# Optimization experiments

Measured on AMD Instinct MI355X. Metric: run time of the kernel, lower is better.

## Reference

```python
import jax, jax.numpy as jnp
import numpy as np

N_AGENTS, OBS_DIM, HID, ACT_DIM = 8192, 64, 128, 16


def setup_inputs() -> dict:
    key = jax.random.key(0)
    k = jax.random.split(key, 8)
    obs_agents = jax.random.normal(k[0], (N_AGENTS, OBS_DIM), dtype=jnp.float32)
    # binary adjacency, {0,1}, int32 (index/mask semantics, non-differentiable)
    adj = jax.random.randint(k[1], (N_AGENTS, N_AGENTS), 0, 2, dtype=jnp.int32)
    def lin(kk, fan_in, fan_out):
        lim = 1.0 / np.sqrt(fan_in)
        kw, kb = jax.random.split(kk)
        W = jax.random.uniform(kw, (fan_in, fan_out), jnp.float32, -lim, lim)
        b = jax.random.uniform(kb, (fan_out,), jnp.float32, -lim, lim)
        return W, b
    W1, b1 = lin(k[2], OBS_DIM, HID)          # encoder
    W2, b2 = lin(k[3], 2 * HID, HID)          # actor layer 1
    W3, b3 = lin(k[4], HID, ACT_DIM)          # actor layer 2
    return {"obs_agents": obs_agents, "adj": adj,
            "W1": W1, "b1": b1, "W2": W2, "b2": b2, "W3": W3, "b3": b3}


def reference(obs_agents, adj, W1, b1, W2, b2, W3, b3):
    # per-agent encode: h = tanh(obs @ W1 + b1)  -> [N, HID]
    h = jnp.tanh(obs_agents @ W1 + b1)
    # neighbor mean message: mean of h[j] over j with adj[i,j]!=0, zeros if no neighbors
    a = adj.astype(h.dtype)                      # [N, N] binary
    deg = jnp.sum(a, axis=1, keepdims=True)      # [N, 1]
    msg = (a @ h) / jnp.maximum(deg, 1.0)        # zero rows stay zero
    # actor MLP on concat([h, msg])
    combined = jnp.concatenate([h, msg], axis=-1)            # [N, 2*HID]
    hid = jnp.tanh(combined @ W2 + b2)                        # [N, HID]
    logits = hid @ W3 + b3                                    # [N, ACT_DIM]
    return logits
```

## Files before the change

### kernel.cpp

```cpp
#include <hip/hip_runtime.h>
#include <stdint.h>
#include <math.h>

#define NAG 8192
#define NB  144
#define BM  128
#define NSPLIT 32
#define LDB 264

typedef __attribute__((ext_vector_type(8))) short short8;
typedef __attribute__((ext_vector_type(4))) float floatx4;

__device__ __forceinline__ float bf2f(unsigned short u) {
    union { uint32_t i; float f; } v; v.i = ((uint32_t)u) << 16; return v.f;
}
__device__ __forceinline__ unsigned short f2bf(float f) {
    union { float f; uint32_t i; } v; v.f = f;
    uint32_t x = v.i;
    return (unsigned short)((x + 0x7FFFu + ((x >> 16) & 1u)) >> 16);
}
__device__ __forceinline__ unsigned short f2h(float f) {
    union { _Float16 h; unsigned short u; } v; v.h = (_Float16)f; return v.u;
}
__device__ __forceinline__ float h2f(unsigned short u) {
    union { _Float16 h; unsigned short u; } v; v.u = u; return (float)v.h;
}

__global__ __launch_bounds__(64) void k0_init(
    int* __restrict__ flag, const unsigned short* __restrict__ W1raw)
{
    int big = 0;
    #pragma unroll
    for (int j = 0; j < 8; ++j) {
        float v = bf2f(W1raw[threadIdx.x * 8 + j]);
        if (!(fabsf(v) <= 1e6f)) big = 1;
    }
    unsigned long long m = __ballot(big);
    if (threadIdx.x == 0) *flag = (m != 0ull) ? 1 : 0;
}

__global__ __launch_bounds__(256) void k1_encode(
    const void* __restrict__ obs,
    const void* __restrict__ W1,
    const void* __restrict__ b1,
    const int* __restrict__ flag,
    float* __restrict__ h_f32,
    unsigned short* __restrict__ hT)
{
    __shared__ float obs_lds[32][68];
    __shared__ unsigned short ht_lds[128][33];
    const int t = threadIdx.x;
    const int abase = blockIdx.x * 32;
    const bool isf = (*flag != 0);

    {
        int a = t >> 3, c0 = (t & 7) * 8;
        if (isf) {
            const float* p = (const float*)obs;
            #pragma unroll
            for (int j = 0; j < 8; ++j)
                obs_lds[a][c0 + j] = p[(size_t)(abase + a) * 64 + c0 + j];
        } else {
            const unsigned short* p = (const unsigned short*)obs;
            #pragma unroll
            for (int j = 0; j < 8; ++j)
                obs_lds[a][c0 + j] = bf2f(p[(size_t)(abase + a) * 64 + c0 + j]);
        }
    }
    __syncthreads();

    const int o = t & 127;
    const int half = t >> 7;
    float acc[16];
    if (isf) {
        const float* Wp = (const float*)W1;
        float bias = ((const float*)b1)[o];
        #pragma unroll
        for (int i = 0; i < 16; ++i) acc[i] = bias;
        for (int k0 = 0; k0 < 64; k0 += 8) {
            float w[8];
            #pragma unroll
            for (int j = 0; j < 8; ++j) w[j] = Wp[(k0 + j) * 128 + o];
            #pragma unroll
            for (int j = 0; j < 8; ++j)
                #pragma unroll
                for (int i = 0; i < 16; ++i)
                    acc[i] = fmaf(obs_lds[half * 16 + i][k0 + j], w[j], acc[i]);
        }
    } else {
        const unsigned short* Wp = (const unsigned short*)W1;
        float bias = bf2f(((const unsigned short*)b1)[o]);
        #pragma unroll
        for (int i = 0; i < 16; ++i) acc[i] = bias;
        for (int k0 = 0; k0 < 64; k0 += 8) {
            float w[8];
            #pragma unroll
            for (int j = 0; j < 8; ++j) w[j] = bf2f(Wp[(k0 + j) * 128 + o]);
            #pragma unroll
            for (int j = 0; j < 8; ++j)
                #pragma unroll
                for (int i = 0; i < 16; ++i)
                    acc[i] = fmaf(obs_lds[half * 16 + i][k0 + j], w[j], acc[i]);
        }
    }
    #pragma unroll
    for (int i = 0; i < 16; ++i) {
        float th = tanhf(acc[i]);
        int a = half * 16 + i;
        h_f32[(size_t)(abase + a) * 128 + o] = th;
        ht_lds[o][a] = f2bf(th);
    }
    __syncthreads();

    for (int p = 0; p < 18; ++p) {
        int n = p * 8 + (t >> 5);
        int a = t & 31;
        unsigned short v;
        if (n < 128)       v = ht_lds[n][a];
        else if (n == 128) v = 0x3F80;
        else               v = 0;
        hT[(size_t)n * NAG + abase + a] = v;
    }
}

__global__ __launch_bounds__(512, 4) void k2_msggemm(
    const int* __restrict__ adj,
    const unsigned short* __restrict__ hT,
    unsigned short* __restrict__ Cp16)
{
    __shared__ __align__(16) unsigned short Blds[144 * LDB];
    const int t = threadIdx.x;
    const int mtile = blockIdx.x & 63;
    const int ks = blockIdx.x >> 6;
    const int row0 = mtile * BM;
    const int kbeg = ks * 256;

    const int wave = t >> 6, lane = t & 63;
    const int fm = lane & 15, quad = lane >> 4;

    #pragma unroll
    for (int i = 0; i < 9; ++i) {
        int idx = i * 512 + t;
        int row = idx >> 5, ch = idx & 31;
        uint4 v = *reinterpret_cast<const uint4*>(hT + (size_t)row * NAG + kbeg + ch * 8);
        *reinterpret_cast<uint4*>(&Blds[row * LDB + ch * 8]) = v;
    }
    __syncthreads();

    floatx4 acc[9];
    #pragma unroll
    for (int i = 0; i < 9; ++i) acc[i] = (floatx4)0.f;

    const int* aP = adj + (size_t)(row0 + wave * 16 + fm) * NAG + kbeg + quad * 8;

    for (int w = 0; w < 8; ++w) {
        int4 v0 = *reinterpret_cast<const int4*>(aP + w * 32);
        int4 v1 = *reinterpret_cast<const int4*>(aP + w * 32 + 4);
        union { uint32_t u[4]; short8 s; } af;
        af.u[0] = ((uint32_t)v0.x | ((uint32_t)v0.y << 16)) * 0x3F80u;
        af.u[1] = ((uint32_t)v0.z | ((uint32_t)v0.w << 16)) * 0x3F80u;
        af.u[2] = ((uint32_t)v1.x | ((uint32_t)v1.y << 16)) * 0x3F80u;
        af.u[3] = ((uint32_t)v1.z | ((uint32_t)v1.w << 16)) * 0x3F80u;
        #pragma unroll
        for (int j = 0; j < 9; ++j) {
            short8 bf = *reinterpret_cast<const short8*>(&Blds[(j * 16 + fm) * LDB + w * 32 + quad * 8]);
            acc[j] = __builtin_amdgcn_mfma_f32_16x16x32_bf16(af.s, bf, acc[j], 0, 0, 0);
        }
    }

    unsigned short* out = Cp16 + (size_t)ks * (NAG * NB);
    #pragma unroll
    for (int j = 0; j < 9; ++j) {
        int col = j * 16 + fm;
        #pragma unroll
        for (int r = 0; r < 4; ++r) {
            int row = row0 + wave * 16 + quad * 4 + r;
            out[(size_t)row * NB + col] = f2h(acc[j][r]);
        }
    }
}

__global__ __launch_bounds__(256) void k3_actor(
    const float* __restrict__ h_f32,
    const unsigned short* __restrict__ Cp16,
    const void* __restrict__ W2,
    const void* __restrict__ b2,
    const void* __restrict__ W3,
    const void* __restrict__ b3,
    const int* __restrict__ flag,
    void* __restrict__ out)
{
    __shared__ float4 comb4[16][66];
    __shared__ float hid[16][132];
    __shared__ float inv_lds[16];
    const int t = threadIdx.x;
    const int abase = blockIdx.x * 16;
    const bool isf = (*flag != 0);
    const size_t PS = (size_t)NAG * NB;

    if (t < 16) {
        float deg = 0.f;
        #pragma unroll
        for (int s = 0; s < NSPLIT; ++s)
            deg += h2f(Cp16[s * PS + (size_t)(abase + t) * NB + 128]);
        inv_lds[t] = 1.0f / fmaxf(deg, 1.0f);
    }
    __syncthreads();

    #pragma unroll
    for (int jj = 0; jj < 4; ++jj) {
        int idx = jj * 256 + t;
        int a = idx >> 6, q = idx & 63;
        float4 v;
        if (q < 32) {
            v = *reinterpret_cast<const float4*>(h_f32 + (size_t)(abase + a) * 128 + q * 4);
        } else {
            int f = (q - 32) * 4;
            float s0 = 0.f, s1 = 0.f, s2 = 0.f, s3 = 0.f;
            #pragma unroll
            for (int s = 0; s < NSPLIT; ++s) {
                ushort4 p = *reinterpret_cast<const ushort4*>(Cp16 + s * PS + (size_t)(abase + a) * NB + f);
                s0 += h2f(p.x); s1 += h2f(p.y); s2 += h2f(p.z); s3 += h2f(p.w);
            }
            float sc = inv_lds[a];
            v = make_float4(s0 * sc, s1 * sc, s2 * sc, s3 * sc);
        }
        comb4[a][q] = v;
    }
    __syncthreads();

    const int o = t & 127, half = t >> 7;
    float acc[8];
    if (isf) {
        const float* Wp = (const float*)W2;
        float bias = ((const float*)b2)[o];
        #pragma unroll
        for (int i = 0; i < 8; ++i) acc[i] = bias;
        for (int cq = 0; cq < 64; ++cq) {
            float w0 = Wp[(cq * 4 + 0) * 128 + o];
            float w1 = Wp[(cq * 4 + 1) * 128 + o];
            float w2 = Wp[(cq * 4 + 2) * 128 + o];
            float w3 = Wp[(cq * 4 + 3) * 128 + o];
            #pragma unroll
            for (int i = 0; i < 8; ++i) {
                float4 v = comb4[half * 8 + i][cq];
                acc[i] = fmaf(v.x, w0, acc[i]);
                acc[i] = fmaf(v.y, w1, acc[i]);
                acc[i] = fmaf(v.z, w2, acc[i]);
                acc[i] = fmaf(v.w, w3, acc[i]);
            }
        }
    } else {
        const unsigned short* Wp = (const unsigned short*)W2;
        float bias = bf2f(((const unsigned short*)b2)[o]);
        #pragma unroll
        for (int i = 0; i < 8; ++i) acc[i] = bias;
        for (int cq = 0; cq < 64; ++cq) {
            float w0 = bf2f(Wp[(cq * 4 + 0) * 128 + o]);
            float w1 = bf2f(Wp[(cq * 4 + 1) * 128 + o]);
            float w2 = bf2f(Wp[(cq * 4 + 2) * 128 + o]);
            float w3 = bf2f(Wp[(cq * 4 + 3) * 128 + o]);
            #pragma unroll
            for (int i = 0; i < 8; ++i) {
                float4 v = comb4[half * 8 + i][cq];
                acc[i] = fmaf(v.x, w0, acc[i]);
                acc[i] = fmaf(v.y, w1, acc[i]);
                acc[i] = fmaf(v.z, w2, acc[i]);
                acc[i] = fmaf(v.w, w3, acc[i]);
            }
        }
    }
    #pragma unroll
    for (int i = 0; i < 8; ++i)
        hid[half * 8 + i][o] = tanhf(acc[i]);
    __syncthreads();

    const int q = t & 15, ar = t >> 4;
    float l;
    if (isf) {
        const float* Wp = (const float*)W3;
        l = ((const float*)b3)[q];
        #pragma unroll 4
        for (int oo = 0; oo < 128; ++oo)
            l = fmaf(hid[ar][oo], Wp[oo * 16 + q], l);
    } else {
        const unsigned short* Wp = (const unsigned short*)W3;
        l = bf2f(((const unsigned short*)b3)[q]);
        #pragma unroll 4
        for (int oo = 0; oo < 128; ++oo)
            l = fmaf(hid[ar][oo], bf2f(Wp[oo * 16 + q]), l);
    }
    size_t i0 = (size_t)(abase + ar) * 16 + q;
    if (isf) ((float*)out)[i0] = l;
    else     ((unsigned short*)out)[i0] = f2bf(l);
}

extern "C" void kernel_launch(void* const* d_in, const int* in_sizes, int n_in,
                              void* d_out, int out_size, void* d_ws, size_t ws_size,
                              hipStream_t stream) {
    const void* obs = d_in[0];
    const int*  adj = (const int*)d_in[1];
    const void* W1  = d_in[2];
    const void* b1  = d_in[3];
    const void* W2  = d_in[4];
    const void* b2  = d_in[5];
    const void* W3  = d_in[6];
    const void* b3  = d_in[7];

    char* ws = (char*)d_ws;
    unsigned short* hT   = (unsigned short*)(ws);
    float*          h_f32= (float*)(ws + 2359296);
    unsigned short* Cp16 = (unsigned short*)(ws + 6553600);
    int*            flag = (int*)(ws + 82051072);

    hipLaunchKernelGGL(k0_init, dim3(1), dim3(64), 0, stream, flag, (const unsigned short*)W1);
    hipLaunchKernelGGL(k1_encode, dim3(256), dim3(256), 0, stream, obs, W1, b1, flag, h_f32, hT);
    hipLaunchKernelGGL(k2_msggemm, dim3(2048), dim3(512), 0, stream, adj, hT, Cp16);
    hipLaunchKernelGGL(k3_actor, dim3(512), dim3(256), 0, stream, h_f32, Cp16, W2, b2, W3, b3, flag, d_out);
}
```

Baseline: 457.8 us.

## Stage adjacency tile in LDS and stream hT from global in msg GEMM

Swaps which operand of the adjacency-times-h GEMM is staged in shared memory. The int32 adjacency tile is now loaded coalesced, converted to bf16 and stored in LDS, while the hT operand is read directly from global memory (cached) per MFMA. The M tile halves to 64 rows with 256-thread blocks, doubling the grid, to cut LDS size and raise occupancy. The change trades a coalesced adj load for uncoalesced per-lane global reads of hT that are repeated across blocks.

```diff
diff --git a/kernel.cpp b/kernel.cpp
--- a/kernel.cpp
+++ b/kernel.cpp
@@ -4,9 +4,10 @@
 
 #define NAG 8192
 #define NB  144
-#define BM  128
+#define BM  64
+#define BK  256
 #define NSPLIT 32
-#define LDB 264
+#define LDA 264
 
 typedef __attribute__((ext_vector_type(8))) short short8;
 typedef __attribute__((ext_vector_type(4))) float floatx4;
@@ -123,27 +124,30 @@
     }
 }
 
-__global__ __launch_bounds__(512, 4) void k2_msggemm(
+__global__ __launch_bounds__(256, 4) void k2_msggemm(
     const int* __restrict__ adj,
     const unsigned short* __restrict__ hT,
     unsigned short* __restrict__ Cp16)
 {
-    __shared__ __align__(16) unsigned short Blds[144 * LDB];
+    __shared__ __align__(16) unsigned short Alds[BM * LDA];
     const int t = threadIdx.x;
-    const int mtile = blockIdx.x & 63;
-    const int ks = blockIdx.x >> 6;
+    const int mtile = blockIdx.x & 127;
+    const int ks = blockIdx.x >> 7;
     const int row0 = mtile * BM;
     const int kbeg = ks * 256;
 
     const int wave = t >> 6, lane = t & 63;
     const int fm = lane & 15, quad = lane >> 4;
 
-    #pragma unroll
-    for (int i = 0; i < 9; ++i) {
-        int idx = i * 512 + t;
-        int row = idx >> 5, ch = idx & 31;
-        uint4 v = *reinterpret_cast<const uint4*>(hT + (size_t)row * NAG + kbeg + ch * 8);
-        *reinterpret_cast<uint4*>(&Blds[row * LDB + ch * 8]) = v;
+    {
+        const int* src = adj + (size_t)(row0 + wave * 16) * NAG + kbeg + lane * 4;
+        #pragma unroll 8
+        for (int n = 0; n < 16; ++n) {
+            int4 v = *reinterpret_cast<const int4*>(src + (size_t)n * NAG);
+            uint32_t d0 = ((uint32_t)v.x | ((uint32_t)v.y << 16)) * 0x3F80u;
+            uint32_t d1 = ((uint32_t)v.z | ((uint32_t)v.w << 16)) * 0x3F80u;
+            *reinterpret_cast<uint2*>(&Alds[(wave * 16 + n) * LDA + lane * 4]) = make_uint2(d0, d1);
+        }
     }
     __syncthreads();
 
@@ -151,20 +155,14 @@
     #pragma unroll
     for (int i = 0; i < 9; ++i) acc[i] = (floatx4)0.f;
 
-    const int* aP = adj + (size_t)(row0 + wave * 16 + fm) * NAG + kbeg + quad * 8;
+    const unsigned short* bP = hT + (size_t)fm * NAG + kbeg + quad * 8;
 
     for (int w = 0; w < 8; ++w) {
-        int4 v0 = *reinterpret_cast<const int4*>(aP + w * 32);
-        int4 v1 = *reinterpret_cast<const int4*>(aP + w * 32 + 4);
-        union { uint32_t u[4]; short8 s; } af;
-        af.u[0] = ((uint32_t)v0.x | ((uint32_t)v0.y << 16)) * 0x3F80u;
-        af.u[1] = ((uint32_t)v0.z | ((uint32_t)v0.w << 16)) * 0x3F80u;
-        af.u[2] = ((uint32_t)v1.x | ((uint32_t)v1.y << 16)) * 0x3F80u;
-        af.u[3] = ((uint32_t)v1.z | ((uint32_t)v1.w << 16)) * 0x3F80u;
+        short8 af = *reinterpret_cast<const short8*>(&Alds[(wave * 16 + fm) * LDA + w * 32 + quad * 8]);
         #pragma unroll
         for (int j = 0; j < 9; ++j) {
-            short8 bf = *reinterpret_cast<const short8*>(&Blds[(j * 16 + fm) * LDB + w * 32 + quad * 8]);
-            acc[j] = __builtin_amdgcn_mfma_f32_16x16x32_bf16(af.s, bf, acc[j], 0, 0, 0);
+            short8 bf = *reinterpret_cast<const short8*>(bP + (size_t)(j * 16) * NAG + w * 32);
+            acc[j] = __builtin_amdgcn_mfma_f32_16x16x32_bf16(af, bf, acc[j], 0, 0, 0);
         }
     }
 
@@ -315,6 +313,6 @@
 
     hipLaunchKernelGGL(k0_init, dim3(1), dim3(64), 0, stream, flag, (const unsigned short*)W1);
     hipLaunchKernelGGL(k1_encode, dim3(256), dim3(256), 0, stream, obs, W1, b1, flag, h_f32, hT);
-    hipLaunchKernelGGL(k2_msggemm, dim3(2048), dim3(512), 0, stream, adj, hT, Cp16);
+    hipLaunchKernelGGL(k2_msggemm, dim3(4096), dim3(256), 0, stream, adj, hT, Cp16);
     hipLaunchKernelGGL(k3_actor, dim3(512), dim3(256), 0, stream, h_f32, Cp16, W2, b2, W3, b3, flag, d_out);
 }
```

Result: slower. 513.2 us (+12.1%).

## Pack adjacency into bitmask and rebalance split-K message GEMM

Applied to the files above, without the earlier changes.

A new kernel reads the int32 adjacency once with coalesced loads and compresses it into 64-bit ballot bitmasks. The message GEMM then reads these bits and expands them into bf16 operands in registers, instead of loading strided int4 rows of adjacency. Split-K drops from 32 to 8, with 64-row tiles and four inner staging passes through LDS, which shrinks the fp16 partial buffer that the actor kernel has to reduce. The cost is an extra kernel launch, an extra bitmask round trip through memory, more barriers and more hT re-staging inside each block.

```diff
diff --git a/kernel.cpp b/kernel.cpp
--- a/kernel.cpp
+++ b/kernel.cpp
@@ -4,8 +4,7 @@
 
 #define NAG 8192
 #define NB  144
-#define BM  128
-#define NSPLIT 32
+#define NSPLIT 8
 #define LDB 264
 
 typedef __attribute__((ext_vector_type(8))) short short8;
@@ -37,6 +36,28 @@
     }
     unsigned long long m = __ballot(big);
     if (threadIdx.x == 0) *flag = (m != 0ull) ? 1 : 0;
+}
+
+__global__ __launch_bounds__(256) void kp_pack(
+    const int* __restrict__ adj, unsigned long long* __restrict__ bits)
+{
+    const int lane = threadIdx.x & 63;
+    const int gw = blockIdx.x * 4 + (threadIdx.x >> 6);
+    for (int it = 0; it < 32; ++it) {
+        size_t u = ((size_t)it * 8192 + gw) * 4;
+        size_t col = u * 64 + lane;
+        unsigned long long m0, m1, m2, m3;
+        m0 = __ballot(adj[col]         != 0);
+        m1 = __ballot(adj[col + 64]    != 0);
+        m2 = __ballot(adj[col + 128]   != 0);
+        m3 = __ballot(adj[col + 192]   != 0);
+        if (lane == 0) {
+            bits[u]     = m0;
+            bits[u + 1] = m1;
+            bits[u + 2] = m2;
+            bits[u + 3] = m3;
+        }
+    }
 }
 
 __global__ __launch_bounds__(256) void k1_encode(
@@ -123,48 +144,56 @@
     }
 }
 
-__global__ __launch_bounds__(512, 4) void k2_msggemm(
-    const int* __restrict__ adj,
+__global__ __launch_bounds__(256, 2) void k2_msggemm(
+    const uint32_t* __restrict__ bits,
     const unsigned short* __restrict__ hT,
     unsigned short* __restrict__ Cp16)
 {
     __shared__ __align__(16) unsigned short Blds[144 * LDB];
     const int t = threadIdx.x;
-    const int mtile = blockIdx.x & 63;
-    const int ks = blockIdx.x >> 6;
-    const int row0 = mtile * BM;
-    const int kbeg = ks * 256;
+    const int mtile = blockIdx.x & 127;
+    const int ks = blockIdx.x >> 7;
+    const int row0 = mtile * 64;
+    const int kbeg = ks * 1024;
 
     const int wave = t >> 6, lane = t & 63;
     const int fm = lane & 15, quad = lane >> 4;
 
-    #pragma unroll
-    for (int i = 0; i < 9; ++i) {
-        int idx = i * 512 + t;
-        int row = idx >> 5, ch = idx & 31;
-        uint4 v = *reinterpret_cast<const uint4*>(hT + (size_t)row * NAG + kbeg + ch * 8);
-        *reinterpret_cast<uint4*>(&Blds[row * LDB + ch * 8]) = v;
-    }
-    __syncthreads();
-
     floatx4 acc[9];
     #pragma unroll
     for (int i = 0; i < 9; ++i) acc[i] = (floatx4)0.f;
 
-    const int* aP = adj + (size_t)(row0 + wave * 16 + fm) * NAG + kbeg + quad * 8;
-
-    for (int w = 0; w < 8; ++w) {
-        int4 v0 = *reinterpret_cast<const int4*>(aP + w * 32);
-        int4 v1 = *reinterpret_cast<const int4*>(aP + w * 32 + 4);
-        union { uint32_t u[4]; short8 s; } af;
-        af.u[0] = ((uint32_t)v0.x | ((uint32_t)v0.y << 16)) * 0x3F80u;
-        af.u[1] = ((uint32_t)v0.z | ((uint32_t)v0.w << 16)) * 0x3F80u;
-        af.u[2] = ((uint32_t)v1.x | ((uint32_t)v1.y << 16)) * 0x3F80u;
-        af.u[3] = ((uint32_t)v1.z | ((uint32_t)v1.w << 16)) * 0x3F80u;
-        #pragma unroll
-        for (int j = 0; j < 9; ++j) {
-            short8 bf = *reinterpret_cast<const short8*>(&Blds[(j * 16 + fm) * LDB + w * 32 + quad * 8]);
-            acc[j] = __builtin_amdgcn_mfma_f32_16x16x32_bf16(af.s, bf, acc[j], 0, 0, 0);
+    const int arow = row0 + wave * 16 + fm;
+    const uint32_t* aWp = bits + (size_t)arow * 256 + (kbeg >> 5);
+
+    for (int ss = 0; ss < 4; ++ss) {
+        if (ss) __syncthreads();
+        #pragma unroll 9
+        for (int i = 0; i < 18; ++i) {
+            int idx = i * 256 + t;
+            int row = idx >> 5, ch = idx & 31;
+            uint4 v = *reinterpret_cast<const uint4*>(hT + (size_t)row * NAG + kbeg + ss * 256 + ch * 8);
+            *reinterpret_cast<uint4*>(&Blds[row * LDB + ch * 8]) = v;
+        }
+        int4 a0 = *reinterpret_cast<const int4*>(aWp + ss * 8);
+        int4 a1 = *reinterpret_cast<const int4*>(aWp + ss * 8 + 4);
+        uint32_t aw[8] = {(uint32_t)a0.x, (uint32_t)a0.y, (uint32_t)a0.z, (uint32_t)a0.w,
+                          (uint32_t)a1.x, (uint32_t)a1.y, (uint32_t)a1.z, (uint32_t)a1.w};
+        __syncthreads();
+        #pragma unroll
+        for (int kw = 0; kw < 8; ++kw) {
+            uint32_t b = (aw[kw] >> (quad * 8)) & 0xFFu;
+            union { uint32_t u[4]; short8 s; } af;
+            #pragma unroll
+            for (int p = 0; p < 4; ++p) {
+                uint32_t bb = b >> (2 * p);
+                af.u[p] = ((bb & 1u) | ((bb & 2u) << 15)) * 0x3F80u;
+            }
+            #pragma unroll
+            for (int j = 0; j < 9; ++j) {
+                short8 bf = *reinterpret_cast<const short8*>(&Blds[(j * 16 + fm) * LDB + kw * 32 + quad * 8]);
+                acc[j] = __builtin_amdgcn_mfma_f32_16x16x32_bf16(af.s, bf, acc[j], 0, 0, 0);
+            }
         }
     }
 
@@ -311,10 +340,13 @@
     unsigned short* hT   = (unsigned short*)(ws);
     float*          h_f32= (float*)(ws + 2359296);
     unsigned short* Cp16 = (unsigned short*)(ws + 6553600);
-    int*            flag = (int*)(ws + 82051072);
+    unsigned long long* bits = (unsigned long long*)(ws + 25427968);
+    int*            flag = (int*)(ws + 33816576);
 
     hipLaunchKernelGGL(k0_init, dim3(1), dim3(64), 0, stream, flag, (const unsigned short*)W1);
+    hipLaunchKernelGGL(kp_pack, dim3(2048), dim3(256), 0, stream, adj, bits);
     hipLaunchKernelGGL(k1_encode, dim3(256), dim3(256), 0, stream, obs, W1, b1, flag, h_f32, hT);
-    hipLaunchKernelGGL(k2_msggemm, dim3(2048), dim3(512), 0, stream, adj, hT, Cp16);
+    hipLaunchKernelGGL(k2_msggemm, dim3(1024), dim3(256), 0, stream,
+                       (const uint32_t*)bits, hT, Cp16);
     hipLaunchKernelGGL(k3_actor, dim3(512), dim3(256), 0, stream, h_f32, Cp16, W2, b2, W3, b3, flag, d_out);
 }
```

Measured after the change: 459.6 us. Within noise of the previous version (+0.4%).
